# Kernel optimization log

Measured on AMD Instinct MI355X. Metric: run time of the kernel, lower is better.

Reference implementation:

```python
import jax, jax.numpy as jnp
import numpy as np

EMBED_DIM = 1024
NUM_HEADS = 16
HEAD_DIM = EMBED_DIM // NUM_HEADS
BATCH = 1
SEQ = 4096


def setup_inputs() -> dict:
    key = jax.random.key(0)
    ks = jax.random.split(key, 9)
    s = 1.0 / np.sqrt(EMBED_DIM)
    inp = {
        "x": jax.random.normal(ks[0], (BATCH, SEQ, EMBED_DIM), dtype=jnp.float32),
        "Wq": jax.random.uniform(ks[1], (EMBED_DIM, EMBED_DIM), jnp.float32, -s, s),
        "bq": jax.random.uniform(ks[2], (EMBED_DIM,), jnp.float32, -s, s),
        "Wk": jax.random.uniform(ks[3], (EMBED_DIM, EMBED_DIM), jnp.float32, -s, s),
        "bk": jax.random.uniform(ks[4], (EMBED_DIM,), jnp.float32, -s, s),
        "Wv": jax.random.uniform(ks[5], (EMBED_DIM, EMBED_DIM), jnp.float32, -s, s),
        "bv": jax.random.uniform(ks[6], (EMBED_DIM,), jnp.float32, -s, s),
        "Wo": jax.random.uniform(ks[7], (EMBED_DIM, EMBED_DIM), jnp.float32, -s, s),
        "bo": jax.random.uniform(ks[8], (EMBED_DIM,), jnp.float32, -s, s),
    }
    return inp


def _attention(x, Wq, bq, Wk, bk, Wv, bv, Wo, bo):
    B, S, E = x.shape
    # project and split heads: [B, H, S, D]
    def split_heads(t):
        return t.reshape(B, S, NUM_HEADS, HEAD_DIM).transpose(0, 2, 1, 3)
    q = split_heads(x @ Wq + bq)
    k = split_heads(x @ Wk + bk)
    v = split_heads(x @ Wv + bv)
    scale = 1.0 / np.sqrt(HEAD_DIM).astype(np.float32)
    # scores: [B, H, S, S] (torch code materializes these per query chunk;
    # math is identical computed in one shot)
    scores = jnp.einsum("bhqd,bhkd->bhqk", q, k) * scale
    attn = jax.nn.softmax(scores, axis=-1)  # dropout p=0 -> identity
    out = jnp.einsum("bhqk,bhkd->bhqd", attn, v)
    out = out.transpose(0, 2, 1, 3).reshape(B, S, E)
    return out @ Wo + bo


def reference(x, Wq, bq, Wk, bk, Wv, bv, Wo, bo):
    return _attention(x, Wq, bq, Wk, bk, Wv, bv, Wo, bo)
```

## Files before the change

kernel.cpp:

```cpp
#include <hip/hip_runtime.h>
#include <stdint.h>

typedef __bf16 bf16;
typedef __bf16 bf16x2 __attribute__((ext_vector_type(2)));
typedef __bf16 bf16x8 __attribute__((ext_vector_type(8)));
typedef float f32x4 __attribute__((ext_vector_type(4)));
typedef float f32x16 __attribute__((ext_vector_type(16)));
typedef uint32_t u32x2 __attribute__((ext_vector_type(2)));

#define EMB 1024
#define SEQ 4096
#define NH 16
#define HD 64

__device__ __forceinline__ void glds16(const void* g, void* l) {
    __builtin_amdgcn_global_load_lds(
        (const __attribute__((address_space(1))) uint32_t*)(uintptr_t)g,
        (__attribute__((address_space(3))) uint32_t*)(uintptr_t)l,
        16, 0, 0);
}

union PU { bf16x2 h; uint32_t u; };
__device__ __forceinline__ uint32_t pack_bf16(float a, float b) {
    PU p; p.h = (bf16x2){(bf16)a, (bf16)b}; return p.u;
}
union FU { bf16x8 v; uint32_t u[4]; };

template<int NT>
__device__ __forceinline__ void transpose_tile(const float* in, bf16* out,
                                               int R, int C, int rbase, int cbase,
                                               bf16* tile ) {
    const int t = threadIdx.x;
    constexpr int PASSES = 512 / NT;
#pragma unroll
    for (int p = 0; p < PASSES; ++p) {
        int idx = t + p * NT;
        int r = idx >> 3;
        int seg = idx & 7;
        const float* src = in + (size_t)(rbase + r) * C + cbase + seg * 8;
        f32x4 a = *(const f32x4*)src;
        f32x4 b = *(const f32x4*)(src + 4);
#pragma unroll
        for (int i = 0; i < 4; ++i) {
            tile[r * 81 + seg * 8 + i]     = (bf16)a[i];
            tile[r * 81 + seg * 8 + 4 + i] = (bf16)b[i];
        }
    }
    __syncthreads();
#pragma unroll
    for (int p = 0; p < PASSES; ++p) {
        int idx = t + p * NT;
        int r = idx >> 3;
        int seg = idx & 7;
        bf16x8 v;
#pragma unroll
        for (int i = 0; i < 8; ++i) v[i] = tile[(seg * 8 + i) * 81 + r];
        *(bf16x8*)(out + (size_t)(cbase + r) * R + rbase + seg * 8) = v;
    }
}

__global__ __launch_bounds__(256) void prep_k(const float* __restrict__ W0,
                                              const float* __restrict__ W1,
                                              const float* __restrict__ W2,
                                              bf16* __restrict__ o0,
                                              bf16* __restrict__ o1,
                                              bf16* __restrict__ o2,
                                              const float* __restrict__ x,
                                              bf16* __restrict__ xb) {
    __shared__ bf16 tile[64 * 81];
    if (blockIdx.z < 3) {
        const float* in = blockIdx.z == 0 ? W0 : (blockIdx.z == 1 ? W1 : W2);
        bf16* out = blockIdx.z == 0 ? o0 : (blockIdx.z == 1 ? o1 : o2);
        transpose_tile<256>(in, out, EMB, EMB, blockIdx.y * 64, blockIdx.x * 64, tile);
    } else {
        size_t linear = blockIdx.y * 16 + blockIdx.x;
#pragma unroll
        for (int i = 0; i < 4; ++i) {
            size_t base = linear * 16384 + (size_t)i * 4096 + threadIdx.x * 16;
#pragma unroll
            for (int h = 0; h < 2; ++h) {
                f32x4 a = *(const f32x4*)(x + base + h * 8);
                f32x4 b = *(const f32x4*)(x + base + h * 8 + 4);
                bf16x8 v;
#pragma unroll
                for (int j = 0; j < 4; ++j) { v[j] = (bf16)a[j]; v[4 + j] = (bf16)b[j]; }
                *(bf16x8*)(xb + base + h * 8) = v;
            }
        }
    }
}

__global__ __launch_bounds__(256) void transpose_k(const float* __restrict__ in,
                                                   bf16* __restrict__ out,
                                                   int R, int C) {
    __shared__ bf16 tile[64 * 81];
    transpose_tile<256>(in, out, R, C, blockIdx.y * 64, blockIdx.x * 64, tile);
}

template<bool A_BF16, bool FUSED>
__global__ __launch_bounds__(256, 3) void gemm_m97(
    const void* __restrict__ A,
    const bf16* __restrict__ Wt0, const bf16* __restrict__ Wt1,
    const bf16* __restrict__ Wt2,
    const float* __restrict__ b0, const float* __restrict__ b1,
    const float* __restrict__ b2,
    void* __restrict__ out0, void* __restrict__ out1,
    bf16* __restrict__ outVt) {
    constexpr int SMEM_BYTES = A_BF16 ? (FUSED ? 18432 : 16384) : 24576;
    __shared__ __align__(16) uint8_t smem[SMEM_BYTES];
    float* aF = (float*)smem;
    bf16*  aB = (bf16*)smem;
    bf16*  bL = (bf16*)(smem + (A_BF16 ? 8192 : 16384));

    const int t = threadIdx.x;
    const int lane = t & 63;
    const int wave = t >> 6;
    const int l15 = lane & 15;
    const int quad = lane >> 4;
    const int wrow = (wave >> 1) * 64;
    const int wcol = (wave & 1) * 64;
    const int nb = blockIdx.x;
    const int which = FUSED ? (nb >> 3) : 0;
    const int ncol = (FUSED ? (nb & 7) : nb) * 128;
    const int mblock = blockIdx.y * 128;

    const bf16* Wt = FUSED ? (which == 0 ? Wt0 : (which == 1 ? Wt1 : Wt2)) : Wt0;
    const float* bias = FUSED ? (which == 0 ? b0 : (which == 1 ? b1 : b2)) : b0;

    float bv[4];
#pragma unroll
    for (int nt = 0; nt < 4; ++nt) bv[nt] = bias[ncol + wcol + nt * 16 + l15];

    f32x4 acc[4][4];
#pragma unroll
    for (int mt = 0; mt < 4; ++mt)
#pragma unroll
        for (int nt = 0; nt < 4; ++nt) acc[mt][nt] = (f32x4){0.f, 0.f, 0.f, 0.f};

    const int a4row = lane >> 3, a4seg = lane & 7;
    const int b2row = lane >> 2, b2seg = lane & 3;

    for (int k0 = 0; k0 < EMB; k0 += 32) {
        __syncthreads();
        if constexpr (!A_BF16) {
#pragma unroll
            for (int i = 0; i < 4; ++i) {
                int row = i * 32 + wave * 8 + a4row;
                int sg = a4seg ^ (row & 7);
                glds16((const float*)A + (size_t)(mblock + row) * EMB + k0 + sg * 4,
                       smem + i * 4096 + wave * 1024);
            }
        } else {
#pragma unroll
            for (int i = 0; i < 2; ++i) {
                int row = i * 64 + wave * 16 + b2row;
                int sg = b2seg ^ ((row >> 1) & 3);
                glds16((const bf16*)A + (size_t)(mblock + row) * EMB + k0 + sg * 8,
                       smem + i * 4096 + wave * 1024);
            }
        }
#pragma unroll
        for (int i = 0; i < 2; ++i) {
            int row = i * 64 + wave * 16 + b2row;
            int sg = b2seg ^ ((row >> 1) & 3);
            glds16(Wt + (size_t)(ncol + row) * EMB + k0 + sg * 8,
                   (uint8_t*)bL + i * 4096 + wave * 1024);
        }
        __syncthreads();

        bf16x8 af[4], bfr[4];
#pragma unroll
        for (int mt = 0; mt < 4; ++mt) {
            int rl = wrow + mt * 16 + l15;
            if constexpr (!A_BF16) {
                f32x4 lo = *(const f32x4*)(aF + rl * 32 + ((2 * quad)     ^ (rl & 7)) * 4);
                f32x4 hi = *(const f32x4*)(aF + rl * 32 + ((2 * quad + 1) ^ (rl & 7)) * 4);
#pragma unroll
                for (int j = 0; j < 4; ++j) {
                    af[mt][j]     = (bf16)lo[j];
                    af[mt][4 + j] = (bf16)hi[j];
                }
            } else {
                af[mt] = *(const bf16x8*)(aB + rl * 32 + (quad ^ ((rl >> 1) & 3)) * 8);
            }
        }
#pragma unroll
        for (int nt = 0; nt < 4; ++nt) {
            int rl = wcol + nt * 16 + l15;
            bfr[nt] = *(const bf16x8*)(bL + rl * 32 + (quad ^ ((rl >> 1) & 3)) * 8);
        }
#pragma unroll
        for (int mt = 0; mt < 4; ++mt)
#pragma unroll
            for (int nt = 0; nt < 4; ++nt)
                acc[mt][nt] = __builtin_amdgcn_mfma_f32_16x16x32_bf16(
                    af[mt], bfr[nt], acc[mt][nt], 0, 0, 0);
    }

    if (!FUSED || which < 2) {
        void* outp = FUSED ? (which == 0 ? out0 : out1) : out0;
#pragma unroll
        for (int mt = 0; mt < 4; ++mt)
#pragma unroll
            for (int nt = 0; nt < 4; ++nt)
#pragma unroll
                for (int r = 0; r < 4; ++r) {
                    size_t row = mblock + wrow + mt * 16 + quad * 4 + r;
                    size_t col = ncol + wcol + nt * 16 + l15;
                    float v = acc[mt][nt][r] + bv[nt];
                    if constexpr (FUSED) ((bf16*)outp)[row * EMB + col] = (bf16)v;
                    else                 ((float*)outp)[row * EMB + col] = v;
                }
    } else if constexpr (FUSED) {
        __syncthreads();
        bf16* tr = (bf16*)smem + wave * 2304;
#pragma unroll
        for (int ch = 0; ch < 2; ++ch) {
#pragma unroll
            for (int mt = 0; mt < 4; ++mt)
#pragma unroll
                for (int ntl = 0; ntl < 2; ++ntl)
#pragma unroll
                    for (int r = 0; r < 4; ++r) {
                        int d_local = ntl * 16 + l15;
                        int s_local = mt * 16 + quad * 4 + r;
                        int nt = 2 * ch + ntl;
                        tr[d_local * 72 + s_local] = (bf16)(acc[mt][nt][r] + bv[nt]);
                    }
            int d2 = lane & 31, h2 = lane >> 5;
#pragma unroll
            for (int j = 0; j < 4; ++j) {
                bf16x8 v = *(const bf16x8*)(tr + d2 * 72 + h2 * 32 + j * 8);
                *(bf16x8*)(outVt + (size_t)(ncol + wcol + ch * 32 + d2) * SEQ +
                           mblock + wrow + h2 * 32 + j * 8) = v;
            }
        }
    }
}

__global__ __launch_bounds__(256, 3) void attn_k(bf16* __restrict__ QO,
                                                 const bf16* __restrict__ Km,
                                                 const bf16* __restrict__ Vt,
                                                 const float* __restrict__ Wo,
                                                 bf16* __restrict__ wt_o) {
    __shared__ bf16 k_lds[2][64 * 64];
    __shared__ bf16 v_lds[2][64 * 64];

    if (blockIdx.y == NH) {
        bf16* tile = &k_lds[0][0];
#pragma unroll 1
        for (int i = 0; i < 8; ++i) {
            int tid = blockIdx.x * 8 + i;
            int ty = tid >> 4, tx = tid & 15;
            transpose_tile<256>(Wo, wt_o, EMB, EMB, ty * 64, tx * 64, tile);
            __syncthreads();
        }
        return;
    }

    const int t = threadIdx.x;
    const int lane = t & 63;
    const int wave = t >> 6;
    const int l31 = lane & 31;
    const int hi = lane >> 5;
    const int l7 = lane & 7;
    const int head = blockIdx.y;
    const int qbase = blockIdx.x * 128 + wave * 32;
    const float QSCALE = 0.125f * 1.4426950408889634f;

    const int srow = wave * 16 + (lane >> 3);
    const int ssg  = lane & 7;

    bf16x8 qf[4];
#pragma unroll
    for (int s = 0; s < 4; ++s) {
        bf16x8 raw = *(const bf16x8*)(QO + (size_t)(qbase + l31) * EMB +
                                      head * HD + s * 16 + hi * 8);
#pragma unroll
        for (int j = 0; j < 8; ++j) qf[s][j] = (bf16)((float)raw[j] * QSCALE);
    }

    f32x16 o_acc[2];
#pragma unroll
    for (int db = 0; db < 2; ++db)
#pragma unroll
        for (int z = 0; z < 16; ++z) o_acc[db][z] = 0.f;
    float l_run = 0.f;

#define STAGE(buf, kbv)                                                               \
    do {                                                                              \
        _Pragma("unroll")                                                             \
        for (int i = 0; i < 2; ++i) {                                                 \
            int rr = srow + i * 8;                                                    \
            int sg = ssg ^ (rr & 7);                                                  \
            glds16(Km + (size_t)((kbv) + rr) * EMB + head * HD + sg * 8,              \
                   &k_lds[buf][(wave * 16 + i * 8) * 64]);                            \
            glds16(Vt + (size_t)(head * HD + rr) * SEQ + (kbv) + sg * 8,              \
                   &v_lds[buf][(wave * 16 + i * 8) * 64]);                            \
        }                                                                             \
    } while (0)

#define COMPUTE(buf)                                                                  \
    do {                                                                              \
        _Pragma("unroll")                                                             \
        for (int b = 0; b < 2; ++b) {                                                 \
            f32x16 sa;                                                               \
            _Pragma("unroll")                                                         \
            for (int z = 0; z < 16; ++z) sa[z] = 0.f;                                 \
            _Pragma("unroll")                                                         \
            for (int s = 0; s < 4; ++s) {                                             \
                bf16x8 kf = *(const bf16x8*)&k_lds[buf][(32 * b + l31) * 64 +         \
                                (((2 * s + hi) ^ l7) * 8)];                           \
                sa = __builtin_amdgcn_mfma_f32_32x32x16_bf16(kf, qf[s], sa, 0, 0, 0); \
            }                                                                         \
            uint32_t u0[4], u1[4];                                                    \
            _Pragma("unroll")                                                         \
            for (int i = 0; i < 4; ++i) {                                             \
                float p0 = __builtin_amdgcn_exp2f(sa[4 * i + 0]);                     \
                float p1 = __builtin_amdgcn_exp2f(sa[4 * i + 1]);                     \
                float p2 = __builtin_amdgcn_exp2f(sa[4 * i + 2]);                     \
                float p3 = __builtin_amdgcn_exp2f(sa[4 * i + 3]);                     \
                l_run += (p0 + p1) + (p2 + p3);                                       \
                u0[i] = pack_bf16(p0, p1);                                            \
                u1[i] = pack_bf16(p2, p3);                                            \
            }                                                                         \
            _Pragma("unroll")                                                         \
            for (int sp = 0; sp < 2; ++sp) {                                          \
                u32x2 ra = __builtin_amdgcn_permlane32_swap(u0[2 * sp], u0[2 * sp + 1], false, false); \
                u32x2 rb = __builtin_amdgcn_permlane32_swap(u1[2 * sp], u1[2 * sp + 1], false, false); \
                FU A;                                                                 \
                A.u[0] = ra[0]; A.u[1] = rb[0]; A.u[2] = ra[1]; A.u[3] = rb[1];       \
                int tt = 2 * b + sp;                                                  \
                _Pragma("unroll")                                                     \
                for (int db = 0; db < 2; ++db) {                                      \
                    bf16x8 vf = *(const bf16x8*)&v_lds[buf][(db * 32 + l31) * 64 +    \
                                    (((2 * tt + hi) ^ l7) * 8)];                      \
                    o_acc[db] = __builtin_amdgcn_mfma_f32_32x32x16_bf16(              \
                        A.v, vf, o_acc[db], 0, 0, 0);                                 \
                }                                                                     \
            }                                                                         \
        }                                                                             \
    } while (0)

    STAGE(0, 0);
    for (int kb = 0; kb < SEQ; kb += 128) {
        __syncthreads();
        STAGE(1, kb + 64);
        COMPUTE(0);
        __syncthreads();
        if (kb + 128 < SEQ) STAGE(0, kb + 128);
        COMPUTE(1);
    }
#undef STAGE
#undef COMPUTE

    l_run += __shfl_xor(l_run, 32);
    float inv = 1.0f / l_run;
    float invr[16];
#pragma unroll
    for (int reg = 0; reg < 16; ++reg)
        invr[reg] = __shfl(inv, (reg & 3) + 8 * (reg >> 2) + 4 * hi);
#pragma unroll
    for (int db = 0; db < 2; ++db)
#pragma unroll
        for (int reg = 0; reg < 16; ++reg) {
            int q = (reg & 3) + 8 * (reg >> 2) + 4 * hi;
            QO[(size_t)(qbase + q) * EMB + head * HD + db * 32 + l31] =
                (bf16)(o_acc[db][reg] * invr[reg]);
        }
}

extern "C" void kernel_launch(void* const* d_in, const int* in_sizes, int n_in,
                              void* d_out, int out_size, void* d_ws, size_t ws_size,
                              hipStream_t stream) {
    const float* x  = (const float*)d_in[0];
    const float* Wq = (const float*)d_in[1];
    const float* bq = (const float*)d_in[2];
    const float* Wk = (const float*)d_in[3];
    const float* bk = (const float*)d_in[4];
    const float* Wv = (const float*)d_in[5];
    const float* bv = (const float*)d_in[6];
    const float* Wo = (const float*)d_in[7];
    const float* bo = (const float*)d_in[8];

    const size_t MAT = (size_t)SEQ * EMB;
    const size_t WMT = (size_t)EMB * EMB;

    bf16* o16   = (bf16*)d_out;
    bf16* Wt_q  = o16;
    bf16* Wt_k  = o16 + WMT;
    bf16* Wt_v  = o16 + 2 * WMT;
    bf16* Vtb   = o16 + 3 * WMT;

    bf16* wsb   = (bf16*)d_ws;
    bf16* QOb   = wsb;
    bf16* Kb    = wsb + MAT;
    bf16* xb    = wsb + 2 * MAT;

    dim3 blk(256);
    dim3 gP(16, 16, 4);
    dim3 gF(24, SEQ / 128);
    dim3 gO(EMB / 128, SEQ / 128);

    if (ws_size >= 3 * MAT * sizeof(bf16)) {
        prep_k<<<gP, blk, 0, stream>>>(Wq, Wk, Wv, Wt_q, Wt_k, Wt_v, x, xb);

        gemm_m97<true, true><<<gF, blk, 0, stream>>>(
            xb, Wt_q, Wt_k, Wt_v, bq, bk, bv, QOb, Kb, Vtb);

        dim3 gA(SEQ / 128, NH + 1);
        attn_k<<<gA, blk, 0, stream>>>(QOb, Kb, Vtb, Wo, xb);

        gemm_m97<true, false><<<gO, blk, 0, stream>>>(
            QOb, xb, nullptr, nullptr, bo, nullptr, nullptr, d_out, nullptr, nullptr);
    } else {
        bf16* Wt_o = wsb + MAT;
        dim3 gTW(EMB / 64, EMB / 64);
        transpose_k<<<gTW, blk, 0, stream>>>(Wq, Wt_q, EMB, EMB);
        transpose_k<<<gTW, blk, 0, stream>>>(Wk, Wt_k, EMB, EMB);
        transpose_k<<<gTW, blk, 0, stream>>>(Wv, Wt_v, EMB, EMB);
        gemm_m97<false, true><<<gF, blk, 0, stream>>>(
            x, Wt_q, Wt_k, Wt_v, bq, bk, bv, QOb, Kb, Vtb);
        dim3 gA(SEQ / 128, NH);
        attn_k<<<gA, blk, 0, stream>>>(QOb, Kb, Vtb, nullptr, nullptr);
        transpose_k<<<gTW, blk, 0, stream>>>(Wo, Wt_o, EMB, EMB);
        gemm_m97<true, false><<<gO, blk, 0, stream>>>(
            QOb, Wt_o, nullptr, nullptr, bo, nullptr, nullptr, d_out, nullptr, nullptr);
    }
}
```

Baseline: 232.1 us.

## Fold Wo transpose into attention tail and batch MFMAs with priority hints

The extra row of attention blocks that transposed Wo is removed. Instead, the first 256 attention blocks each transpose one 64x64 Wo tile after writing their output, so the transpose no longer needs dedicated blocks. The attention inner loop is restructured so both QK^T MFMA chains are issued back to back, then the softmax exponentials, then the PV MFMAs, with s_setprio raising wave priority around the MFMA bursts. The occupancy hint drops from 3 to 2 blocks per CU, which gives the compiler more registers but may reduce latency hiding.

```diff
diff --git a/kernel.cpp b/kernel.cpp
--- a/kernel.cpp
+++ b/kernel.cpp
@@ -238,25 +238,13 @@
     }
 }
 
-__global__ __launch_bounds__(256, 3) void attn_k(bf16* __restrict__ QO,
+__global__ __launch_bounds__(256, 2) void attn_k(bf16* __restrict__ QO,
                                                  const bf16* __restrict__ Km,
                                                  const bf16* __restrict__ Vt,
                                                  const float* __restrict__ Wo,
                                                  bf16* __restrict__ wt_o) {
     __shared__ bf16 k_lds[2][64 * 64];
     __shared__ bf16 v_lds[2][64 * 64];
-
-    if (blockIdx.y == NH) {
-        bf16* tile = &k_lds[0][0];
-#pragma unroll 1
-        for (int i = 0; i < 8; ++i) {
-            int tid = blockIdx.x * 8 + i;
-            int ty = tid >> 4, tx = tid & 15;
-            transpose_tile<256>(Wo, wt_o, EMB, EMB, ty * 64, tx * 64, tile);
-            __syncthreads();
-        }
-        return;
-    }
 
     const int t = threadIdx.x;
     const int lane = t & 63;
@@ -302,44 +290,53 @@
 
 #define COMPUTE(buf)                                                                  \
     do {                                                                              \
+        f32x16 sa[2];                                                                 \
         _Pragma("unroll")                                                             \
-        for (int b = 0; b < 2; ++b) {                                                 \
-            f32x16 sa;                                                               \
+        for (int b = 0; b < 2; ++b)                                                   \
             _Pragma("unroll")                                                         \
-            for (int z = 0; z < 16; ++z) sa[z] = 0.f;                                 \
-            _Pragma("unroll")                                                         \
-            for (int s = 0; s < 4; ++s) {                                             \
-                bf16x8 kf = *(const bf16x8*)&k_lds[buf][(32 * b + l31) * 64 +         \
-                                (((2 * s + hi) ^ l7) * 8)];                           \
-                sa = __builtin_amdgcn_mfma_f32_32x32x16_bf16(kf, qf[s], sa, 0, 0, 0); \
-            }                                                                         \
-            uint32_t u0[4], u1[4];                                                    \
+            for (int z = 0; z < 16; ++z) sa[b][z] = 0.f;                              \
+        __builtin_amdgcn_s_setprio(1);                                                \
+        _Pragma("unroll")                                                             \
+        for (int s = 0; s < 4; ++s) {                                                 \
+            bf16x8 kf0 = *(const bf16x8*)&k_lds[buf][(l31) * 64 +                     \
+                            (((2 * s + hi) ^ l7) * 8)];                               \
+            bf16x8 kf1 = *(const bf16x8*)&k_lds[buf][(32 + l31) * 64 +                \
+                            (((2 * s + hi) ^ l7) * 8)];                               \
+            sa[0] = __builtin_amdgcn_mfma_f32_32x32x16_bf16(kf0, qf[s], sa[0], 0, 0, 0);\
+            sa[1] = __builtin_amdgcn_mfma_f32_32x32x16_bf16(kf1, qf[s], sa[1], 0, 0, 0);\
+        }                                                                             \
+        __builtin_amdgcn_s_setprio(0);                                                \
+        uint32_t u0[2][4], u1[2][4];                                                  \
+        _Pragma("unroll")                                                             \
+        for (int b = 0; b < 2; ++b)                                                   \
             _Pragma("unroll")                                                         \
             for (int i = 0; i < 4; ++i) {                                             \
-                float p0 = __builtin_amdgcn_exp2f(sa[4 * i + 0]);                     \
-                float p1 = __builtin_amdgcn_exp2f(sa[4 * i + 1]);                     \
-                float p2 = __builtin_amdgcn_exp2f(sa[4 * i + 2]);                     \
-                float p3 = __builtin_amdgcn_exp2f(sa[4 * i + 3]);                     \
+                float p0 = __builtin_amdgcn_exp2f(sa[b][4 * i + 0]);                  \
+                float p1 = __builtin_amdgcn_exp2f(sa[b][4 * i + 1]);                  \
+                float p2 = __builtin_amdgcn_exp2f(sa[b][4 * i + 2]);                  \
+                float p3 = __builtin_amdgcn_exp2f(sa[b][4 * i + 3]);                  \
                 l_run += (p0 + p1) + (p2 + p3);                                       \
-                u0[i] = pack_bf16(p0, p1);                                            \
-                u1[i] = pack_bf16(p2, p3);                                            \
+                u0[b][i] = pack_bf16(p0, p1);                                         \
+                u1[b][i] = pack_bf16(p2, p3);                                         \
             }                                                                         \
-            _Pragma("unroll")                                                         \
-            for (int sp = 0; sp < 2; ++sp) {                                          \
-                u32x2 ra = __builtin_amdgcn_permlane32_swap(u0[2 * sp], u0[2 * sp + 1], false, false); \
-                u32x2 rb = __builtin_amdgcn_permlane32_swap(u1[2 * sp], u1[2 * sp + 1], false, false); \
-                FU A;                                                                 \
-                A.u[0] = ra[0]; A.u[1] = rb[0]; A.u[2] = ra[1]; A.u[3] = rb[1];       \
-                int tt = 2 * b + sp;                                                  \
-                _Pragma("unroll")                                                     \
-                for (int db = 0; db < 2; ++db) {                                      \
-                    bf16x8 vf = *(const bf16x8*)&v_lds[buf][(db * 32 + l31) * 64 +    \
-                                    (((2 * tt + hi) ^ l7) * 8)];                      \
-                    o_acc[db] = __builtin_amdgcn_mfma_f32_32x32x16_bf16(              \
-                        A.v, vf, o_acc[db], 0, 0, 0);                                 \
-                }                                                                     \
-            }                                                                         \
+        __builtin_amdgcn_s_setprio(1);                                                \
+        _Pragma("unroll")                                                             \
+        for (int tt = 0; tt < 4; ++tt) {                                              \
+            const int b = tt >> 1, sp = tt & 1;                                       \
+            u32x2 ra = __builtin_amdgcn_permlane32_swap(                              \
+                u0[b][2 * sp], u0[b][2 * sp + 1], false, false);                      \
+            u32x2 rb = __builtin_amdgcn_permlane32_swap(                              \
+                u1[b][2 * sp], u1[b][2 * sp + 1], false, false);                      \
+            FU A;                                                                     \
+            A.u[0] = ra[0]; A.u[1] = rb[0]; A.u[2] = ra[1]; A.u[3] = rb[1];           \
+            bf16x8 vf0 = *(const bf16x8*)&v_lds[buf][(l31) * 64 +                     \
+                            (((2 * tt + hi) ^ l7) * 8)];                              \
+            bf16x8 vf1 = *(const bf16x8*)&v_lds[buf][(32 + l31) * 64 +                \
+                            (((2 * tt + hi) ^ l7) * 8)];                              \
+            o_acc[0] = __builtin_amdgcn_mfma_f32_32x32x16_bf16(A.v, vf0, o_acc[0], 0, 0, 0);\
+            o_acc[1] = __builtin_amdgcn_mfma_f32_32x32x16_bf16(A.v, vf1, o_acc[1], 0, 0, 0);\
         }                                                                             \
+        __builtin_amdgcn_s_setprio(0);                                                \
     } while (0)
 
     STAGE(0, 0);
@@ -368,6 +365,16 @@
             QO[(size_t)(qbase + q) * EMB + head * HD + db * 32 + l31] =
                 (bf16)(o_acc[db][reg] * invr[reg]);
         }
+
+    if (Wo != nullptr) {
+        int bid = blockIdx.y * gridDim.x + blockIdx.x;
+        if (bid < 256) {
+            __syncthreads();
+            bf16* tile = &k_lds[0][0];
+            int ty = bid >> 4, tx = bid & 15;
+            transpose_tile<256>(Wo, wt_o, EMB, EMB, ty * 64, tx * 64, tile);
+        }
+    }
 }
 
 extern "C" void kernel_launch(void* const* d_in, const int* in_sizes, int n_in,
@@ -408,7 +415,7 @@
         gemm_m97<true, true><<<gF, blk, 0, stream>>>(
             xb, Wt_q, Wt_k, Wt_v, bq, bk, bv, QOb, Kb, Vtb);
 
-        dim3 gA(SEQ / 128, NH + 1);
+        dim3 gA(SEQ / 128, NH);
         attn_k<<<gA, blk, 0, stream>>>(QOb, Kb, Vtb, Wo, xb);
 
         gemm_m97<true, false><<<gO, blk, 0, stream>>>(
```

New measurement: 228.2 us. No clear change (-1.7%).
